# Kernel optimization log

Hardware: AMD Instinct MI355X
Metric: run time of the kernel (lower is better)

The kernel has to match this reference:

```python
import jax, jax.numpy as jnp
import numpy as np

N_NODES = 100000
NNZ = 1600000
IN_CH = 256
OUT_CH = 64  # heads * out_channels, heads=1


def setup_inputs() -> dict:
    key = jax.random.key(0)
    k1, k2, k3, k4, k5 = jax.random.split(key, 5)
    X = jax.random.normal(k1, (N_NODES, IN_CH), dtype=jnp.float32)
    # nn.Linear(in, heads*out, bias=False) weight: [out, in]
    W_lin = jax.random.normal(k2, (OUT_CH, IN_CH), dtype=jnp.float32) * (1.0 / np.sqrt(IN_CH))
    # sparse Laplacian L in COO form
    L_rows = jax.random.randint(k3, (NNZ,), 0, N_NODES, dtype=jnp.int64)
    L_cols = jax.random.randint(k4, (NNZ,), 0, N_NODES, dtype=jnp.int64)
    L_vals = jax.random.uniform(k5, (NNZ,), dtype=jnp.float32)
    return {"g1": 0, "g2": 0, "X": X, "W_lin": W_lin,
            "L_rows": L_rows, "L_cols": L_cols, "L_vals": L_vals}


def reference(g1, g2, X, W_lin, L_rows, L_cols, L_vals):
    # dense projection: X @ W^T  -> [N, out]
    Xp = jnp.einsum('ni,oi->no', X, W_lin)
    # SpMM: Xv = L @ Xp, COO gather-scale-scatter
    gathered = L_vals[:, None] * Xp[L_cols]            # [nnz, out]
    Xv = jax.ops.segment_sum(gathered, L_rows, num_segments=N_NODES)
    return Xv
```

## Files before the change

### kernel.cpp

```cpp
#include <hip/hip_runtime.h>

#define N_IN_CH 256
#define N_OUT_CH 64
#define XPAD 264
#define BROW 128
#define NBK 1024
#define B1_T 512
#define B1_E 4096
#define ECAP 4096
#define OVFCAP 65536
#define GEMM_GRID 768

typedef __attribute__((ext_vector_type(8))) short short8;
typedef __attribute__((ext_vector_type(4))) float f32x4;

__device__ inline ushort f2bf(float f) {
    unsigned u = __float_as_uint(f);
    return (ushort)((u + 0x7FFFu + ((u >> 16) & 1u)) >> 16);
}
__device__ inline float bf2f(ushort u) {
    return __uint_as_float(((unsigned)u) << 16);
}

__global__ __launch_bounds__(256) void mfma_gemm_kernel(const float* __restrict__ X,
        const float* __restrict__ W, ushort* __restrict__ Xp, int nrows,
        int* __restrict__ zbuf, int nzero) {
    __shared__ ushort Ws[64 * XPAD];
    const int tid = threadIdx.x;

    if (blockIdx.x == 0) {
        for (int i = tid; i < nzero; i += 256) zbuf[i] = 0;
    }

    #pragma unroll
    for (int it = 0; it < 16; ++it) {
        int f = it * 256 + tid;
        int n = f >> 6, c4 = f & 63;
        float4 w = *(const float4*)&W[n * N_IN_CH + c4 * 4];
        ushort4 u;
        u.x = f2bf(w.x); u.y = f2bf(w.y); u.z = f2bf(w.z); u.w = f2bf(w.w);
        *(ushort4*)&Ws[n * XPAD + c4 * 4] = u;
    }
    __syncthreads();

    const int wave = tid >> 6, lane = tid & 63;
    const int ml = lane & 15, q = lane >> 4;
    const int ntiles = (nrows + 15) >> 4;
    const int nw = gridDim.x * 4;
    int t = blockIdx.x * 4 + wave;

    const ushort* wsb = &Ws[ml * XPAD + q * 8];

    float4 raw[16];

#define ISSUE_TILE(tt)                                                     \
    do {                                                                   \
        int gr_ = (tt) * 16 + ml;                                          \
        if (gr_ < nrows) {                                                 \
            const float* xr_ = X + (size_t)gr_ * N_IN_CH + q * 8;          \
            _Pragma("unroll")                                              \
            for (int kt_ = 0; kt_ < 8; ++kt_) {                            \
                raw[2 * kt_]     = *(const float4*)&xr_[kt_ * 32];         \
                raw[2 * kt_ + 1] = *(const float4*)&xr_[kt_ * 32 + 4];     \
            }                                                              \
        } else {                                                           \
            _Pragma("unroll")                                              \
            for (int i_ = 0; i_ < 16; ++i_)                                \
                raw[i_] = make_float4(0.f, 0.f, 0.f, 0.f);                 \
        }                                                                  \
    } while (0)

    if (t < ntiles) ISSUE_TILE(t);

    while (t < ntiles) {
        short8 a[8];
        #pragma unroll
        for (int kt = 0; kt < 8; ++kt) {
            float4 f0 = raw[2 * kt], f1 = raw[2 * kt + 1];
            short8 s;
            s[0] = (short)f2bf(f0.x); s[1] = (short)f2bf(f0.y);
            s[2] = (short)f2bf(f0.z); s[3] = (short)f2bf(f0.w);
            s[4] = (short)f2bf(f1.x); s[5] = (short)f2bf(f1.y);
            s[6] = (short)f2bf(f1.z); s[7] = (short)f2bf(f1.w);
            a[kt] = s;
        }
        int tn = t + nw;
        if (tn < ntiles) ISSUE_TILE(tn);

        #pragma unroll
        for (int nt = 0; nt < 4; ++nt) {
            f32x4 acc = {0.f, 0.f, 0.f, 0.f};
            #pragma unroll
            for (int kt = 0; kt < 8; ++kt) {
                short8 b = *(const short8*)&wsb[nt * 16 * XPAD + kt * 32];
                acc = __builtin_amdgcn_mfma_f32_16x16x32_bf16(a[kt], b, acc, 0, 0, 0);
            }
            #pragma unroll
            for (int reg = 0; reg < 4; ++reg) {
                int gr = t * 16 + q * 4 + reg;
                if (gr < nrows)
                    Xp[(size_t)gr * N_OUT_CH + nt * 16 + ml] = f2bf(acc[reg]);
            }
        }
        t = tn;
    }
#undef ISSUE_TILE
}

__global__ __launch_bounds__(B1_T) void bin_kernel(const int* __restrict__ rows,
        const int* __restrict__ cols, const float* __restrict__ vals,
        int* __restrict__ bcur, int* __restrict__ ovfcnt, int4* __restrict__ ovf,
        int2* __restrict__ colbuf, int nnz, int nb) {
    __shared__ int cnt[NBK];
    __shared__ int base[NBK];
    const int t = threadIdx.x;

    for (int i = t; i < nb; i += B1_T) cnt[i] = 0;
    __syncthreads();

    const int e = blockIdx.x * B1_E + t * 8;
    int nval = nnz - e;
    if (nval > 8) nval = 8;
    if (nval < 0) nval = 0;

    int r[8], c[8]; float v[8];
    if (nval == 8) {
        *(int4*)&r[0] = *(const int4*)&rows[e];
        *(int4*)&r[4] = *(const int4*)&rows[e + 4];
        *(int4*)&c[0] = *(const int4*)&cols[e];
        *(int4*)&c[4] = *(const int4*)&cols[e + 4];
        *(float4*)&v[0] = *(const float4*)&vals[e];
        *(float4*)&v[4] = *(const float4*)&vals[e + 4];
    } else {
        #pragma unroll
        for (int j = 0; j < 8; ++j)
            if (j < nval) { r[j] = rows[e + j]; c[j] = cols[e + j]; v[j] = vals[e + j]; }
    }

    #pragma unroll
    for (int j = 0; j < 8; ++j)
        if (j < nval) atomicAdd(&cnt[r[j] >> 7], 1);
    __syncthreads();

    for (int i = t; i < nb; i += B1_T) {
        int cn = cnt[i];
        base[i] = cn ? atomicAdd(&bcur[i], cn) : 0;
        cnt[i] = 0;
    }
    __syncthreads();

    #pragma unroll
    for (int j = 0; j < 8; ++j) {
        if (j < nval) {
            int b = r[j] >> 7;
            int pib = base[b] + atomicAdd(&cnt[b], 1);
            if (pib < ECAP) {
                int2 cv;
                cv.x = c[j] | ((r[j] & 127) << 17);
                cv.y = __float_as_int(v[j]);
                colbuf[(size_t)b * ECAP + pib] = cv;
            } else {
                int op = atomicAdd(ovfcnt, 1);
                if (op < OVFCAP) {
                    int4 o; o.x = r[j]; o.y = c[j];
                    o.z = __float_as_int(v[j]); o.w = 0;
                    ovf[op] = o;
                }
            }
        }
    }
}

__global__ __launch_bounds__(512) void bspmm_kernel(const int* __restrict__ bcur,
        const int2* __restrict__ colbuf, const ushort* __restrict__ Xp,
        float* __restrict__ out, int nrows) {
    __shared__ int2 ebuf[ECAP];
    __shared__ int rc[BROW];
    __shared__ int rb[BROW + 1];
    const int b = blockIdx.x, t = threadIdx.x;
    const int ne = min(bcur[b], ECAP);
    const int2* cb = colbuf + (size_t)b * ECAP;
    const int row0 = b * BROW;
    const int wave = t >> 6, lane = t & 63;

    if (t < BROW) rc[t] = 0;
    __syncthreads();
    for (int i = t; i < ne; i += 512)
        atomicAdd(&rc[(cb[i].x >> 17) & (BROW - 1)], 1);
    __syncthreads();
    int c0 = (t < BROW) ? rc[t] : 0;
    #pragma unroll
    for (int d = 1; d < BROW; d <<= 1) {
        int a = (t < BROW && t >= d) ? rc[t - d] : 0;
        __syncthreads();
        if (t < BROW) rc[t] += a;
        __syncthreads();
    }
    if (t < BROW) rb[t] = rc[t] - c0;
    if (t == 0) rb[BROW] = ne;
    __syncthreads();
    if (t < BROW) rc[t] = 0;
    __syncthreads();
    for (int i = t; i < ne; i += 512) {
        int2 cv = cb[i];
        int rl = (cv.x >> 17) & (BROW - 1);
        int pos = rb[rl] + atomicAdd(&rc[rl], 1);
        ebuf[pos] = cv;
    }
    __syncthreads();

    const int r0 = wave * 16;
    const int s = rb[r0], e = rb[r0 + 16];
    float accv = 0.f;
    int cur = -1;
    int i = s;
    for (; i + 8 <= e; i += 8) {
        int2 cv[8];
        #pragma unroll
        for (int j = 0; j < 8; ++j) cv[j] = ebuf[i + j];
        float x[8];
        #pragma unroll
        for (int j = 0; j < 8; ++j)
            x[j] = bf2f(Xp[(size_t)(cv[j].x & 0x1FFFF) * N_OUT_CH + lane]);
        #pragma unroll
        for (int j = 0; j < 8; ++j) {
            int rl = (cv[j].x >> 17) & (BROW - 1);
            if (rl != cur) {
                if (cur >= 0) out[(size_t)(row0 + cur) * N_OUT_CH + lane] = accv;
                cur = rl; accv = 0.f;
            }
            accv += __int_as_float(cv[j].y) * x[j];
        }
    }
    for (; i < e; ++i) {
        int2 cv = ebuf[i];
        int rl = (cv.x >> 17) & (BROW - 1);
        if (rl != cur) {
            if (cur >= 0) out[(size_t)(row0 + cur) * N_OUT_CH + lane] = accv;
            cur = rl; accv = 0.f;
        }
        accv += __int_as_float(cv.y) *
                bf2f(Xp[(size_t)(cv.x & 0x1FFFF) * N_OUT_CH + lane]);
    }
    if (cur >= 0) out[(size_t)(row0 + cur) * N_OUT_CH + lane] = accv;

    for (int r = r0; r < r0 + 16; ++r) {
        if (rb[r] == rb[r + 1]) {
            int gr = row0 + r;
            if (gr < nrows) out[(size_t)gr * N_OUT_CH + lane] = 0.f;
        }
    }
}

__global__ __launch_bounds__(256) void ovf_kernel(const int* __restrict__ ovfcnt,
        const int4* __restrict__ ovf, const ushort* __restrict__ Xp,
        float* __restrict__ out) {
    int n = min(ovfcnt[0], OVFCAP);
    int lane = threadIdx.x & 63;
    for (int e = blockIdx.x * 4 + (threadIdx.x >> 6); e < n; e += gridDim.x * 4) {
        int4 v = ovf[e];
        atomicAdd(&out[(size_t)v.x * N_OUT_CH + lane],
                  __int_as_float(v.z) * bf2f(Xp[(size_t)v.y * N_OUT_CH + lane]));
    }
}

__global__ __launch_bounds__(256) void spmm_atomic_kernel(const int* __restrict__ rows,
        const int* __restrict__ cols, const float* __restrict__ vals,
        const ushort* __restrict__ Xp, float* __restrict__ out, int nnz) {
    int t = blockIdx.x * blockDim.x + threadIdx.x;
    int e = t >> 6;
    int c = t & 63;
    if (e < nnz) {
        atomicAdd(&out[(size_t)rows[e] * N_OUT_CH + c],
                  vals[e] * bf2f(Xp[(size_t)cols[e] * N_OUT_CH + c]));
    }
}

extern "C" void kernel_launch(void* const* d_in, const int* in_sizes, int n_in,
                              void* d_out, int out_size, void* d_ws, size_t ws_size,
                              hipStream_t stream) {
    const float* X      = (const float*)d_in[2];
    const float* W      = (const float*)d_in[3];
    const int*   L_rows = (const int*)d_in[4];
    const int*   L_cols = (const int*)d_in[5];
    const float* L_vals = (const float*)d_in[6];
    float* out = (float*)d_out;

    const int nrows = in_sizes[2] / N_IN_CH;
    const int nnz   = in_sizes[4];
    const int nb    = (nrows + BROW - 1) / BROW;

    size_t off_xp  = 0;
    size_t xp_b    = (size_t)nrows * N_OUT_CH * 2;
    size_t off_bc  = off_xp + ((xp_b + 15) & ~(size_t)15);
    size_t off_ov  = off_bc + (((size_t)(nb + 1) * 4 + 15) & ~(size_t)15);
    size_t off_cv  = off_ov + (size_t)OVFCAP * 16;
    size_t need    = off_cv + (size_t)nb * ECAP * 8;

    ushort* Xp = (ushort*)((char*)d_ws + off_xp);
    const bool binned = (ws_size >= need && nb <= NBK);
    int* bcur = (int*)((char*)d_ws + off_bc);

    {
        int ntiles = (nrows + 15) >> 4;
        int grid = GEMM_GRID;
        int maxg = (ntiles + 3) / 4;
        if (grid > maxg) grid = maxg;
        mfma_gemm_kernel<<<grid, 256, 0, stream>>>(X, W, Xp, nrows,
                binned ? bcur : (int*)d_ws, binned ? nb + 1 : 0);
    }

    if (binned) {
        int*  ovfcnt = bcur + nb;
        int4* ovf    = (int4*)((char*)d_ws + off_ov);
        int2* colbuf = (int2*)((char*)d_ws + off_cv);

        bin_kernel<<<(nnz + B1_E - 1) / B1_E, B1_T, 0, stream>>>(L_rows, L_cols, L_vals,
                bcur, ovfcnt, ovf, colbuf, nnz, nb);
        bspmm_kernel<<<nb, 512, 0, stream>>>(bcur, colbuf, Xp, out, nrows);
        ovf_kernel<<<16, 256, 0, stream>>>(ovfcnt, ovf, Xp, out);
    } else {
        hipMemsetAsync(d_out, 0, (size_t)out_size * sizeof(float), stream);
        long long total = (long long)nnz * 64;
        spmm_atomic_kernel<<<(int)((total + 255) / 256), 256, 0, stream>>>(
            L_rows, L_cols, L_vals, Xp, out, nnz);
    }
}
```

Measured before the change: 250.1 us.

## Fuse GEMM and binning into one launch, fold overflow pass into SpMM

Merges the bf16 MFMA projection and the COO binning pass into a single kernel, with blocks split by index into GEMM blocks and binning blocks. The two independent phases can then run concurrently, and one launch is saved. The bin-counter zeroing moves to a memset. The bspmm kernel now register-caches its 8 edges per thread instead of reading colbuf twice, and absorbs the overflow pass: every block scans the whole overflow list and keeps its own rows. That scan adds redundant work if the overflow list is ever non-empty.

```diff
diff --git a/kernel.cpp b/kernel.cpp
--- a/kernel.cpp
+++ b/kernel.cpp
@@ -5,11 +5,11 @@
 #define XPAD 264
 #define BROW 128
 #define NBK 1024
-#define B1_T 512
-#define B1_E 4096
+#define B1_T 256
+#define B1_E 2048
 #define ECAP 4096
 #define OVFCAP 65536
-#define GEMM_GRID 768
+#define NGEMM 512
 
 typedef __attribute__((ext_vector_type(8))) short short8;
 typedef __attribute__((ext_vector_type(4))) float f32x4;
@@ -22,158 +22,154 @@
     return __uint_as_float(((unsigned)u) << 16);
 }
 
-__global__ __launch_bounds__(256) void mfma_gemm_kernel(const float* __restrict__ X,
-        const float* __restrict__ W, ushort* __restrict__ Xp, int nrows,
-        int* __restrict__ zbuf, int nzero) {
-    __shared__ ushort Ws[64 * XPAD];
+__global__ __launch_bounds__(256) void fused_kernel(const float* __restrict__ X,
+        const float* __restrict__ W, ushort* __restrict__ Xp, int nrows, int ngemm,
+        const int* __restrict__ rows, const int* __restrict__ cols,
+        const float* __restrict__ vals, int* __restrict__ bcur,
+        int* __restrict__ ovfcnt, int4* __restrict__ ovf,
+        int2* __restrict__ colbuf, int nnz, int nb) {
+    __shared__ union SM {
+        ushort ws[64 * XPAD];
+        struct { int cnt[NBK]; int base[NBK]; } b;
+    } sm;
     const int tid = threadIdx.x;
 
-    if (blockIdx.x == 0) {
-        for (int i = tid; i < nzero; i += 256) zbuf[i] = 0;
-    }
-
-    #pragma unroll
-    for (int it = 0; it < 16; ++it) {
-        int f = it * 256 + tid;
-        int n = f >> 6, c4 = f & 63;
-        float4 w = *(const float4*)&W[n * N_IN_CH + c4 * 4];
-        ushort4 u;
-        u.x = f2bf(w.x); u.y = f2bf(w.y); u.z = f2bf(w.z); u.w = f2bf(w.w);
-        *(ushort4*)&Ws[n * XPAD + c4 * 4] = u;
-    }
-    __syncthreads();
-
-    const int wave = tid >> 6, lane = tid & 63;
-    const int ml = lane & 15, q = lane >> 4;
-    const int ntiles = (nrows + 15) >> 4;
-    const int nw = gridDim.x * 4;
-    int t = blockIdx.x * 4 + wave;
-
-    const ushort* wsb = &Ws[ml * XPAD + q * 8];
-
-    float4 raw[16];
+    if (blockIdx.x < ngemm) {
+        #pragma unroll
+        for (int it = 0; it < 16; ++it) {
+            int f = it * 256 + tid;
+            int n = f >> 6, c4 = f & 63;
+            float4 w = *(const float4*)&W[n * N_IN_CH + c4 * 4];
+            ushort4 u;
+            u.x = f2bf(w.x); u.y = f2bf(w.y); u.z = f2bf(w.z); u.w = f2bf(w.w);
+            *(ushort4*)&sm.ws[n * XPAD + c4 * 4] = u;
+        }
+        __syncthreads();
+
+        const int wave = tid >> 6, lane = tid & 63;
+        const int ml = lane & 15, q = lane >> 4;
+        const int ntiles = (nrows + 15) >> 4;
+        const int nw = ngemm * 4;
+        int t = blockIdx.x * 4 + wave;
+
+        const ushort* wsb = &sm.ws[ml * XPAD + q * 8];
+
+        float4 raw[16];
 
 #define ISSUE_TILE(tt)                                                     \
-    do {                                                                   \
-        int gr_ = (tt) * 16 + ml;                                          \
-        if (gr_ < nrows) {                                                 \
-            const float* xr_ = X + (size_t)gr_ * N_IN_CH + q * 8;          \
-            _Pragma("unroll")                                              \
-            for (int kt_ = 0; kt_ < 8; ++kt_) {                            \
-                raw[2 * kt_]     = *(const float4*)&xr_[kt_ * 32];         \
-                raw[2 * kt_ + 1] = *(const float4*)&xr_[kt_ * 32 + 4];     \
+        do {                                                               \
+            int gr_ = (tt) * 16 + ml;                                      \
+            if (gr_ < nrows) {                                             \
+                const float* xr_ = X + (size_t)gr_ * N_IN_CH + q * 8;      \
+                _Pragma("unroll")                                          \
+                for (int kt_ = 0; kt_ < 8; ++kt_) {                        \
+                    raw[2 * kt_]     = *(const float4*)&xr_[kt_ * 32];     \
+                    raw[2 * kt_ + 1] = *(const float4*)&xr_[kt_ * 32 + 4]; \
+                }                                                          \
+            } else {                                                       \
+                _Pragma("unroll")                                          \
+                for (int i_ = 0; i_ < 16; ++i_)                            \
+                    raw[i_] = make_float4(0.f, 0.f, 0.f, 0.f);             \
             }                                                              \
-        } else {                                                           \
-            _Pragma("unroll")                                              \
-            for (int i_ = 0; i_ < 16; ++i_)                                \
-                raw[i_] = make_float4(0.f, 0.f, 0.f, 0.f);                 \
-        }                                                                  \
-    } while (0)
-
-    if (t < ntiles) ISSUE_TILE(t);
-
-    while (t < ntiles) {
-        short8 a[8];
-        #pragma unroll
-        for (int kt = 0; kt < 8; ++kt) {
-            float4 f0 = raw[2 * kt], f1 = raw[2 * kt + 1];
-            short8 s;
-            s[0] = (short)f2bf(f0.x); s[1] = (short)f2bf(f0.y);
-            s[2] = (short)f2bf(f0.z); s[3] = (short)f2bf(f0.w);
-            s[4] = (short)f2bf(f1.x); s[5] = (short)f2bf(f1.y);
-            s[6] = (short)f2bf(f1.z); s[7] = (short)f2bf(f1.w);
-            a[kt] = s;
-        }
-        int tn = t + nw;
-        if (tn < ntiles) ISSUE_TILE(tn);
-
-        #pragma unroll
-        for (int nt = 0; nt < 4; ++nt) {
-            f32x4 acc = {0.f, 0.f, 0.f, 0.f};
+        } while (0)
+
+        if (t < ntiles) ISSUE_TILE(t);
+
+        while (t < ntiles) {
+            short8 a[8];
             #pragma unroll
             for (int kt = 0; kt < 8; ++kt) {
-                short8 b = *(const short8*)&wsb[nt * 16 * XPAD + kt * 32];
-                acc = __builtin_amdgcn_mfma_f32_16x16x32_bf16(a[kt], b, acc, 0, 0, 0);
+                float4 f0 = raw[2 * kt], f1 = raw[2 * kt + 1];
+                short8 s;
+                s[0] = (short)f2bf(f0.x); s[1] = (short)f2bf(f0.y);
+                s[2] = (short)f2bf(f0.z); s[3] = (short)f2bf(f0.w);
+                s[4] = (short)f2bf(f1.x); s[5] = (short)f2bf(f1.y);
+                s[6] = (short)f2bf(f1.z); s[7] = (short)f2bf(f1.w);
+                a[kt] = s;
             }
+            int tn = t + nw;
+            if (tn < ntiles) ISSUE_TILE(tn);
+
             #pragma unroll
-            for (int reg = 0; reg < 4; ++reg) {
-                int gr = t * 16 + q * 4 + reg;
-                if (gr < nrows)
-                    Xp[(size_t)gr * N_OUT_CH + nt * 16 + ml] = f2bf(acc[reg]);
-            }
-        }
-        t = tn;
-    }
-#undef ISSUE_TILE
-}
-
-__global__ __launch_bounds__(B1_T) void bin_kernel(const int* __restrict__ rows,
-        const int* __restrict__ cols, const float* __restrict__ vals,
-        int* __restrict__ bcur, int* __restrict__ ovfcnt, int4* __restrict__ ovf,
-        int2* __restrict__ colbuf, int nnz, int nb) {
-    __shared__ int cnt[NBK];
-    __shared__ int base[NBK];
-    const int t = threadIdx.x;
-
-    for (int i = t; i < nb; i += B1_T) cnt[i] = 0;
-    __syncthreads();
-
-    const int e = blockIdx.x * B1_E + t * 8;
-    int nval = nnz - e;
-    if (nval > 8) nval = 8;
-    if (nval < 0) nval = 0;
-
-    int r[8], c[8]; float v[8];
-    if (nval == 8) {
-        *(int4*)&r[0] = *(const int4*)&rows[e];
-        *(int4*)&r[4] = *(const int4*)&rows[e + 4];
-        *(int4*)&c[0] = *(const int4*)&cols[e];
-        *(int4*)&c[4] = *(const int4*)&cols[e + 4];
-        *(float4*)&v[0] = *(const float4*)&vals[e];
-        *(float4*)&v[4] = *(const float4*)&vals[e + 4];
-    } else {
-        #pragma unroll
-        for (int j = 0; j < 8; ++j)
-            if (j < nval) { r[j] = rows[e + j]; c[j] = cols[e + j]; v[j] = vals[e + j]; }
-    }
-
-    #pragma unroll
-    for (int j = 0; j < 8; ++j)
-        if (j < nval) atomicAdd(&cnt[r[j] >> 7], 1);
-    __syncthreads();
-
-    for (int i = t; i < nb; i += B1_T) {
-        int cn = cnt[i];
-        base[i] = cn ? atomicAdd(&bcur[i], cn) : 0;
-        cnt[i] = 0;
-    }
-    __syncthreads();
-
-    #pragma unroll
-    for (int j = 0; j < 8; ++j) {
-        if (j < nval) {
-            int b = r[j] >> 7;
-            int pib = base[b] + atomicAdd(&cnt[b], 1);
-            if (pib < ECAP) {
-                int2 cv;
-                cv.x = c[j] | ((r[j] & 127) << 17);
-                cv.y = __float_as_int(v[j]);
-                colbuf[(size_t)b * ECAP + pib] = cv;
-            } else {
-                int op = atomicAdd(ovfcnt, 1);
-                if (op < OVFCAP) {
-                    int4 o; o.x = r[j]; o.y = c[j];
-                    o.z = __float_as_int(v[j]); o.w = 0;
-                    ovf[op] = o;
+            for (int nt = 0; nt < 4; ++nt) {
+                f32x4 acc = {0.f, 0.f, 0.f, 0.f};
+                #pragma unroll
+                for (int kt = 0; kt < 8; ++kt) {
+                    short8 b = *(const short8*)&wsb[nt * 16 * XPAD + kt * 32];
+                    acc = __builtin_amdgcn_mfma_f32_16x16x32_bf16(a[kt], b, acc, 0, 0, 0);
+                }
+                #pragma unroll
+                for (int reg = 0; reg < 4; ++reg) {
+                    int gr = t * 16 + q * 4 + reg;
+                    if (gr < nrows)
+                        Xp[(size_t)gr * N_OUT_CH + nt * 16 + ml] = f2bf(acc[reg]);
                 }
             }
+            t = tn;
+        }
+#undef ISSUE_TILE
+    } else {
+        for (int i = tid; i < nb; i += B1_T) sm.b.cnt[i] = 0;
+        __syncthreads();
+
+        const int e = (blockIdx.x - ngemm) * B1_E + tid * 8;
+        int nval = nnz - e;
+        if (nval > 8) nval = 8;
+        if (nval < 0) nval = 0;
+
+        int r[8], c[8]; float v[8];
+        if (nval == 8) {
+            *(int4*)&r[0] = *(const int4*)&rows[e];
+            *(int4*)&r[4] = *(const int4*)&rows[e + 4];
+            *(int4*)&c[0] = *(const int4*)&cols[e];
+            *(int4*)&c[4] = *(const int4*)&cols[e + 4];
+            *(float4*)&v[0] = *(const float4*)&vals[e];
+            *(float4*)&v[4] = *(const float4*)&vals[e + 4];
+        } else {
+            #pragma unroll
+            for (int j = 0; j < 8; ++j)
+                if (j < nval) { r[j] = rows[e + j]; c[j] = cols[e + j]; v[j] = vals[e + j]; }
+        }
+
+        #pragma unroll
+        for (int j = 0; j < 8; ++j)
+            if (j < nval) atomicAdd(&sm.b.cnt[r[j] >> 7], 1);
+        __syncthreads();
+
+        for (int i = tid; i < nb; i += B1_T) {
+            int cn = sm.b.cnt[i];
+            sm.b.base[i] = cn ? atomicAdd(&bcur[i], cn) : 0;
+            sm.b.cnt[i] = 0;
+        }
+        __syncthreads();
+
+        #pragma unroll
+        for (int j = 0; j < 8; ++j) {
+            if (j < nval) {
+                int b = r[j] >> 7;
+                int pib = sm.b.base[b] + atomicAdd(&sm.b.cnt[b], 1);
+                if (pib < ECAP) {
+                    int2 cv;
+                    cv.x = c[j] | ((r[j] & 127) << 17);
+                    cv.y = __float_as_int(v[j]);
+                    colbuf[(size_t)b * ECAP + pib] = cv;
+                } else {
+                    int op = atomicAdd(ovfcnt, 1);
+                    if (op < OVFCAP) {
+                        int4 o; o.x = r[j]; o.y = c[j];
+                        o.z = __float_as_int(v[j]); o.w = 0;
+                        ovf[op] = o;
+                    }
+                }
+            }
         }
     }
 }
 
 __global__ __launch_bounds__(512) void bspmm_kernel(const int* __restrict__ bcur,
         const int2* __restrict__ colbuf, const ushort* __restrict__ Xp,
-        float* __restrict__ out, int nrows) {
+        float* __restrict__ out, int nrows, const int* __restrict__ ovfcnt,
+        const int4* __restrict__ ovf) {
     __shared__ int2 ebuf[ECAP];
     __shared__ int rc[BROW];
     __shared__ int rb[BROW + 1];
@@ -183,10 +179,26 @@
     const int row0 = b * BROW;
     const int wave = t >> 6, lane = t & 63;
 
+    int2 ev[8];
+    const int ebase = t * 8;
+    int ecnt = ne - ebase;
+    if (ecnt > 8) ecnt = 8;
+    if (ecnt < 0) ecnt = 0;
+    if (ecnt == 8) {
+        #pragma unroll
+        for (int j = 0; j < 4; ++j)
+            *(int4*)&ev[2 * j] = *(const int4*)&cb[ebase + 2 * j];
+    } else {
+        #pragma unroll
+        for (int j = 0; j < 8; ++j)
+            if (j < ecnt) ev[j] = cb[ebase + j];
+    }
+
     if (t < BROW) rc[t] = 0;
     __syncthreads();
-    for (int i = t; i < ne; i += 512)
-        atomicAdd(&rc[(cb[i].x >> 17) & (BROW - 1)], 1);
+    #pragma unroll
+    for (int j = 0; j < 8; ++j)
+        if (j < ecnt) atomicAdd(&rc[(ev[j].x >> 17) & (BROW - 1)], 1);
     __syncthreads();
     int c0 = (t < BROW) ? rc[t] : 0;
     #pragma unroll
@@ -201,11 +213,13 @@
     __syncthreads();
     if (t < BROW) rc[t] = 0;
     __syncthreads();
-    for (int i = t; i < ne; i += 512) {
-        int2 cv = cb[i];
-        int rl = (cv.x >> 17) & (BROW - 1);
-        int pos = rb[rl] + atomicAdd(&rc[rl], 1);
-        ebuf[pos] = cv;
+    #pragma unroll
+    for (int j = 0; j < 8; ++j) {
+        if (j < ecnt) {
+            int rl = (ev[j].x >> 17) & (BROW - 1);
+            int pos = rb[rl] + atomicAdd(&rc[rl], 1);
+            ebuf[pos] = ev[j];
+        }
     }
     __syncthreads();
 
@@ -250,17 +264,14 @@
             if (gr < nrows) out[(size_t)gr * N_OUT_CH + lane] = 0.f;
         }
     }
-}
-
-__global__ __launch_bounds__(256) void ovf_kernel(const int* __restrict__ ovfcnt,
-        const int4* __restrict__ ovf, const ushort* __restrict__ Xp,
-        float* __restrict__ out) {
+
+    __syncthreads();
     int n = min(ovfcnt[0], OVFCAP);
-    int lane = threadIdx.x & 63;
-    for (int e = blockIdx.x * 4 + (threadIdx.x >> 6); e < n; e += gridDim.x * 4) {
-        int4 v = ovf[e];
-        atomicAdd(&out[(size_t)v.x * N_OUT_CH + lane],
-                  __int_as_float(v.z) * bf2f(Xp[(size_t)v.y * N_OUT_CH + lane]));
+    for (int e2 = wave; e2 < n; e2 += 8) {
+        int4 v = ovf[e2];
+        if ((v.x >> 7) == b)
+            atomicAdd(&out[(size_t)v.x * N_OUT_CH + lane],
+                      __int_as_float(v.z) * bf2f(Xp[(size_t)v.y * N_OUT_CH + lane]));
     }
 }
 
@@ -301,25 +312,24 @@
     const bool binned = (ws_size >= need && nb <= NBK);
     int* bcur = (int*)((char*)d_ws + off_bc);
 
-    {
-        int ntiles = (nrows + 15) >> 4;
-        int grid = GEMM_GRID;
-        int maxg = (ntiles + 3) / 4;
-        if (grid > maxg) grid = maxg;
-        mfma_gemm_kernel<<<grid, 256, 0, stream>>>(X, W, Xp, nrows,
-                binned ? bcur : (int*)d_ws, binned ? nb + 1 : 0);
-    }
+    int ntiles = (nrows + 15) >> 4;
+    int ngemm = NGEMM;
+    int maxg = (ntiles + 3) / 4;
+    if (ngemm > maxg) ngemm = maxg;
 
     if (binned) {
         int*  ovfcnt = bcur + nb;
         int4* ovf    = (int4*)((char*)d_ws + off_ov);
         int2* colbuf = (int2*)((char*)d_ws + off_cv);
-
-        bin_kernel<<<(nnz + B1_E - 1) / B1_E, B1_T, 0, stream>>>(L_rows, L_cols, L_vals,
-                bcur, ovfcnt, ovf, colbuf, nnz, nb);
-        bspmm_kernel<<<nb, 512, 0, stream>>>(bcur, colbuf, Xp, out, nrows);
-        ovf_kernel<<<16, 256, 0, stream>>>(ovfcnt, ovf, Xp, out);
+        int nbin = (nnz + B1_E - 1) / B1_E;
+
+        hipMemsetAsync(bcur, 0, (size_t)(nb + 1) * 4, stream);
+        fused_kernel<<<ngemm + nbin, 256, 0, stream>>>(X, W, Xp, nrows, ngemm,
+                L_rows, L_cols, L_vals, bcur, ovfcnt, ovf, colbuf, nnz, nb);
+        bspmm_kernel<<<nb, 512, 0, stream>>>(bcur, colbuf, Xp, out, nrows, ovfcnt, ovf);
     } else {
+        fused_kernel<<<ngemm, 256, 0, stream>>>(X, W, Xp, nrows, ngemm,
+                nullptr, nullptr, nullptr, nullptr, nullptr, nullptr, nullptr, 0, 0);
         hipMemsetAsync(d_out, 0, (size_t)out_size * sizeof(float), stream);
         long long total = (long long)nnz * 64;
         spmm_atomic_kernel<<<(int)((total + 255) / 256), 256, 0, stream>>>(
```

After: 247.8 us. No clear change (-1.0%).
